# Kernel optimization log

Hardware: AMD Instinct MI355X
Metric: run time of the kernel (lower is better)

Reference implementation:

```python
import jax, jax.numpy as jnp
import numpy as np
from jax import lax

B, R, C = 4, 64, 192          # batch, input_resolution, dim
WN, K = 16, 3                 # ka_win_num, kernel_size
WS = R // 4                   # window_size = R / sqrt(WN) = 16
DN = ('NCHW', 'OIHW', 'NCHW')


def setup_inputs() -> dict:
    key = jax.random.key(0)
    ks = jax.random.split(key, 12)
    rn = lambda k, shp, s=0.05: jax.random.normal(k, shp, dtype=jnp.float32) * s
    return {
        'x': jax.random.normal(ks[0], (B, R * R, C), dtype=jnp.float32),
        'conv1_w': rn(ks[1], (WN * C, 1, K, K), 0.1),
        'dc_w': rn(ks[2], (WN, C)),                             # grouped 1x1 (WN*C -> WN)
        'dc_b': jnp.zeros((WN,), jnp.float32),
        'l1_w': rn(ks[3], (4 * WN, WN)),
        'l1_b': jnp.zeros((4 * WN,), jnp.float32),
        'l2_w': rn(ks[4], (WN, 4 * WN)),
        'l2_b': jnp.zeros((WN,), jnp.float32),
        'gk_w': rn(ks[5], (WN,)),                               # 1x1 conv WN -> 1
        'gk_b': jnp.zeros((1,), jnp.float32),
        'fusion_w': rn(ks[6], (C, (WN + 1) * C)),               # 1x1 conv (WN+1)*C -> C
        'fusion_b': jnp.zeros((C,), jnp.float32),
    }


def _forward(x, conv1_w, dc_w, dc_b, l1_w, l1_b, l2_w, l2_b, gk_w, gk_b,
             fusion_w, fusion_b):
    # pad_feature_map is a no-op since R % WS == 0.
    xw = x.reshape(B, R // WS, WS, R // WS, WS, C)
    xw = xw.transpose(0, 1, 3, 5, 2, 4).reshape(B, WN * C, WS, WS)

    # convlayer1: depthwise conv over all WN*C channels
    y = lax.conv_general_dilated(xw, conv1_w, (1, 1), [(1, 1), (1, 1)],
                                 dimension_numbers=DN,
                                 feature_group_count=WN * C)  # (B, WN*C, WS, WS)

    # WinKernel_Reweight: pool -> grouped 1x1 -> gelu -> 1x1 -> sigmoid
    pooled = y.mean(axis=(2, 3)).reshape(B, WN, C)
    w = jnp.einsum('bwc,wc->bw', pooled, dc_w) + dc_b          # downchannel (groups=WN)
    w = jax.nn.gelu(w @ l1_w.T + l1_b, approximate=False)      # (B, 4*WN)
    w = jax.nn.sigmoid(w @ l2_w.T + l2_b)                      # (B, WN)

    kern = conv1_w.reshape(WN, C, K, K)
    kern = w[:, :, None, None, None] * kern[None]              # (B, WN, C, K, K)

    # global kernel: 1x1 conv across the WN axis
    gk = jnp.einsum('bwcij,w->bcij', kern, gk_w) + gk_b[0]     # (B, C, K, K)
    all_k = jnp.concatenate([kern, gk[:, None]], axis=1)       # (B, WN+1, C, K, K)

    # dynamic depthwise conv on the full map, per sample
    xf = x.reshape(B, R, R, C).transpose(0, 3, 1, 2)           # (B, C, R, R)
    xrep = jnp.tile(xf, (1, WN + 1, 1, 1))                     # (B, (WN+1)*C, R, R)
    kflat = all_k.reshape(B, (WN + 1) * C, 1, K, K)

    def dw(xi, ki):  # xi: ((WN+1)*C, R, R), ki: ((WN+1)*C, 1, K, K)
        return lax.conv_general_dilated(xi[None], ki, (1, 1), [(1, 1), (1, 1)],
                                        dimension_numbers=DN,
                                        feature_group_count=(WN + 1) * C)[0]

    out = jax.vmap(dw)(xrep, kflat)                            # (B, (WN+1)*C, R, R)

    # fusion 1x1 conv -> (B, C, R, R) -> (B, L, C)
    out = jnp.einsum('bdhw,cd->bhwc', out, fusion_w) + fusion_b
    return out.reshape(B, R * R, C)


def reference(x, conv1_w, dc_w, dc_b, l1_w, l1_b, l2_w, l2_b, gk_w, gk_b,
              fusion_w, fusion_b):
    return _forward(x, conv1_w, dc_w, dc_b, l1_w, l1_b, l2_w, l2_b,
                    gk_w, gk_b, fusion_w, fusion_b)
```

## Files before the change

kernel.cpp:

```cpp
#include <hip/hip_runtime.h>
#include <hip/hip_bf16.h>
#include <math.h>

#define B_  4
#define R_  64
#define C_  192
#define WN_ 16


typedef __attribute__((ext_vector_type(8))) short short8;
typedef __attribute__((ext_vector_type(4))) float floatx4;

static __device__ __forceinline__ unsigned short f2bf(float f) {
    union { float f; unsigned u; } v; v.f = f;
    unsigned r = v.u + 0x7fffu + ((v.u >> 16) & 1u);
    return (unsigned short)(r >> 16);
}

__global__ __launch_bounds__(256) void pre_kernel(
        const float* __restrict__ x,
        const float* __restrict__ conv1_w,
        const float* __restrict__ dc_w,
        float* __restrict__ w0,
        unsigned short* __restrict__ xfrag,
        float* __restrict__ cw_t) {
    __shared__ float part[3];
    int blk = blockIdx.x;
    int tid = threadIdx.x;

    if (blk < 64) {
        int b = blk >> 4, win = blk & 15;
        int wr = win >> 2, wc = win & 3;
        if (tid < 192) {
            int c = tid;
            const float* xb = x + ((size_t)b * 4096) * C_ + c;
            float Wsum = 0.f, Rtop = 0.f, Rbot = 0.f, Cleft = 0.f, Cright = 0.f;
            float c00 = 0.f, c0F = 0.f, cF0 = 0.f, cFF = 0.f;
            for (int ph = 0; ph < 16; ++ph) {
                int h = wr * 16 + ph;
                #pragma unroll
                for (int pw = 0; pw < 16; ++pw) {
                    int w = wc * 16 + pw;
                    float v = xb[((size_t)(h * 64 + w)) * C_];
                    Wsum += v;
                    if (ph == 0)  { Rtop += v; if (pw == 0) c00 = v; if (pw == 15) c0F = v; }
                    if (ph == 15) { Rbot += v; if (pw == 0) cF0 = v; if (pw == 15) cFF = v; }
                    if (pw == 0)  Cleft  += v;
                    if (pw == 15) Cright += v;
                }
            }
            const float* kp = conv1_w + ((size_t)(win * C_ + c)) * 9;
            float pooled = 0.f;
            #pragma unroll
            for (int i = 0; i < 3; ++i) {
                #pragma unroll
                for (int j = 0; j < 3; ++j) {
                    int di = i - 1, dj = j - 1;
                    float S = Wsum;
                    if (di == -1) S -= Rbot;   else if (di == 1) S -= Rtop;
                    if (dj == -1) S -= Cright; else if (dj == 1) S -= Cleft;
                    if (di == -1 && dj == -1) S += cFF;
                    if (di == -1 && dj ==  1) S += cF0;
                    if (di ==  1 && dj == -1) S += c0F;
                    if (di ==  1 && dj ==  1) S += c00;
                    pooled += kp[i * 3 + j] * S;
                }
            }
            float val = (pooled * (1.f / 256.f)) * dc_w[win * C_ + c];
            for (int off = 32; off; off >>= 1) val += __shfl_down(val, off, 64);
            if ((tid & 63) == 0) part[tid >> 6] = val;
        }
        __syncthreads();
        if (tid == 0) w0[blk] = part[0] + part[1] + part[2];
    } else if (blk < 328) {
        int rb = blk - 64;
        int b = rb / 66, row = rb % 66;
        int h = row - 1;
        unsigned short* orow = xfrag + (size_t)rb * 12672;
        for (int c = tid; c < 1584; c += 256) {
            int kc = c / 264;
            int rc = c - kc * 264;
            int px = rc >> 2;
            int cio = (rc & 3) * 8;
            int w = px - 1;
            short8 o;
            if (h >= 0 && h < 64 && w >= 0 && w < 64) {
                const float* src = x + (((size_t)b * 4096) + h * 64 + w) * C_ + kc * 32 + cio;
                const float4 v0 = *(const float4*)(src);
                const float4 v1 = *(const float4*)(src + 4);
                o[0] = (short)f2bf(v0.x); o[1] = (short)f2bf(v0.y);
                o[2] = (short)f2bf(v0.z); o[3] = (short)f2bf(v0.w);
                o[4] = (short)f2bf(v1.x); o[5] = (short)f2bf(v1.y);
                o[6] = (short)f2bf(v1.z); o[7] = (short)f2bf(v1.w);
            } else {
                o = (short8){0,0,0,0,0,0,0,0};
            }
            *(short8*)(orow + (size_t)c * 8) = o;
        }
    } else {
        int base = (blk - 328) * 512 + tid * 2;
        #pragma unroll
        for (int e = 0; e < 2; ++e) {
            int o = base + e;
            int t = o / 3072;
            int r = o - t * 3072;
            cw_t[o] = conv1_w[(size_t)r * 9 + t];
        }
    }
}

__global__ __launch_bounds__(192) void weff_kernel(
        const float* __restrict__ cw_t,
        const float* __restrict__ gk_w,
        const float* __restrict__ gk_b,
        const float* __restrict__ fusion_w,
        const float* __restrict__ w0,
        const float* __restrict__ dc_b,
        const float* __restrict__ l1_w,
        const float* __restrict__ l1_b,
        const float* __restrict__ l2_w,
        const float* __restrict__ l2_b,
        unsigned short* __restrict__ Wl) {
    __shared__ float hbuf[64];
    __shared__ float s_sh[16];
    int blk = blockIdx.x;
    int b = blk / C_, co = blk % C_;
    int tid = threadIdx.x;

    if (tid < 64) {
        float a = l1_b[tid];
        #pragma unroll
        for (int w = 0; w < 16; ++w)
            a += (w0[b * 16 + w] + dc_b[w]) * l1_w[tid * 16 + w];
        hbuf[tid] = 0.5f * a * (1.f + erff(a * 0.70710678118654752f));
    }
    __syncthreads();
    if (tid < 16) {
        float a2 = l2_b[tid];
        #pragma unroll
        for (int k = 0; k < 64; ++k) a2 += hbuf[k] * l2_w[tid * 64 + k];
        s_sh[tid] = 1.f / (1.f + expf(-a2));
    }
    __syncthreads();

    int ci = tid;
    float fg = fusion_w[(size_t)co * 3264 + 16 * C_ + ci];
    float acc[9];
    float g0 = fg * gk_b[0];
    #pragma unroll
    for (int t = 0; t < 9; ++t) acc[t] = g0;
    for (int w = 0; w < 16; ++w) {
        float coef = (fusion_w[(size_t)co * 3264 + w * C_ + ci] + fg * gk_w[w]) * s_sh[w];
        #pragma unroll
        for (int t = 0; t < 9; ++t)
            acc[t] += coef * cw_t[t * 3072 + w * C_ + ci];
    }
    #pragma unroll
    for (int t = 0; t < 9; ++t) {
        int kc = ci >> 5, cio = ci & 31;
        Wl[((((size_t)(b * 9 + t)) * 6 + kc) * C_ + co) * 32 + cio] = f2bf(acc[t]);
    }
}

__global__ __launch_bounds__(256, 1) void conv_kernel(
        const unsigned short* __restrict__ xfrag,
        const unsigned short* __restrict__ Wl,
        const float* __restrict__ fusion_b,
        float* __restrict__ out) {
    const int h = blockIdx.x >> 2;
    const int b = blockIdx.x & 3;
    const int tid = threadIdx.x;
    const int wv = tid >> 6;
    const int lane = tid & 63;
    const int lo = lane & 15, quad = lane >> 4;
    const int n0 = wv * 48;

    const short* xp = (const short*)xfrag;
    const short* wp = (const short*)Wl;

    int Abase[4], Bbase[3];
    #pragma unroll
    for (int mt = 0; mt < 4; ++mt)
        Abase[mt] = (b * 66 + h + 1) * 12672 + (mt * 16 + lo + 1) * 32 + quad * 8;
    #pragma unroll
    for (int nt = 0; nt < 3; ++nt)
        Bbase[nt] = (b * 9 * 6 * C_ + n0 + nt * 16 + lo) * 32 + quad * 8;

    floatx4 acc[4][3];
    #pragma unroll
    for (int mt = 0; mt < 4; ++mt)
        #pragma unroll
        for (int nt = 0; nt < 3; ++nt)
            acc[mt][nt] = (floatx4){0.f, 0.f, 0.f, 0.f};

    short8 Ab[3][4];
    short8 Bb[3][3];

    auto load_step = [&](int s, int slot) {
        const int tap = s / 6, kc = s % 6;
        const int dh = tap / 3 - 1, dw = tap % 3 - 1;
        const int aoff = dh * 12672 + dw * 32 + kc * 2112;
        const int boff = (tap * 6 + kc) * (C_ * 32);
        #pragma unroll
        for (int mt = 0; mt < 4; ++mt)
            Ab[slot][mt] = *(const short8*)(xp + Abase[mt] + aoff);
        #pragma unroll
        for (int nt = 0; nt < 3; ++nt)
            Bb[slot][nt] = *(const short8*)(wp + Bbase[nt] + boff);
    };

    load_step(0, 0);
    load_step(1, 1);

    #pragma unroll
    for (int step = 0; step < 54; ++step) {
        const int cur = step % 3;
        if (step + 2 < 54) load_step(step + 2, (step + 2) % 3);
        #pragma unroll
        for (int mt = 0; mt < 4; ++mt)
            #pragma unroll
            for (int nt = 0; nt < 3; ++nt)
                acc[mt][nt] = __builtin_amdgcn_mfma_f32_16x16x32_bf16(
                    Ab[cur][mt], Bb[cur][nt], acc[mt][nt], 0, 0, 0);
    }

    #pragma unroll
    for (int nt = 0; nt < 3; ++nt) {
        const int co = n0 + nt * 16 + lo;
        const float fb = fusion_b[co];
        #pragma unroll
        for (int mt = 0; mt < 4; ++mt) {
            #pragma unroll
            for (int r = 0; r < 4; ++r) {
                const int pix = mt * 16 + quad * 4 + r;
                out[(((size_t)b * 4096) + h * 64 + pix) * C_ + co] = acc[mt][nt][r] + fb;
            }
        }
    }
}

extern "C" void kernel_launch(void* const* d_in, const int* in_sizes, int n_in,
                              void* d_out, int out_size, void* d_ws, size_t ws_size,
                              hipStream_t stream) {
    const float* x        = (const float*)d_in[0];
    const float* conv1_w  = (const float*)d_in[1];
    const float* dc_w     = (const float*)d_in[2];
    const float* dc_b     = (const float*)d_in[3];
    const float* l1_w     = (const float*)d_in[4];
    const float* l1_b     = (const float*)d_in[5];
    const float* l2_w     = (const float*)d_in[6];
    const float* l2_b     = (const float*)d_in[7];
    const float* gk_w     = (const float*)d_in[8];
    const float* gk_b     = (const float*)d_in[9];
    const float* fusion_w = (const float*)d_in[10];
    const float* fusion_b = (const float*)d_in[11];
    float* out = (float*)d_out;

    char* ws = (char*)d_ws;
    float* w0   = (float*)ws;
    float* cw_t = (float*)(ws + 512);
    unsigned short* Wl    = (unsigned short*)(ws + 512 + 110592);
    unsigned short* xfrag = (unsigned short*)(ws + 512 + 110592 + 2654208);

    hipLaunchKernelGGL(pre_kernel, dim3(382), dim3(256), 0, stream,
                       x, conv1_w, dc_w, w0, xfrag, cw_t);
    hipLaunchKernelGGL(weff_kernel, dim3(B_ * C_), dim3(192), 0, stream,
                       cw_t, gk_w, gk_b, fusion_w, w0, dc_b, l1_w, l1_b, l2_w, l2_b, Wl);
    hipLaunchKernelGGL(conv_kernel, dim3(R_ * B_), dim3(256), 0, stream,
                       xfrag, Wl, fusion_b, out);
}
```

Before: 126.6 us.

## Fuse bf16 input staging into conv kernel via LDS and split pooling blocks

Removes the padded bf16 xfrag workspace that pre_kernel wrote, so the conv kernel now converts three input rows from fp32 to bf16 into shared memory itself, in two channel phases. The conv block grows to 512 threads, with 8 waves split across pixel halves and channel groups, and a swizzled block-to-row mapping. The window pooling is split across 4x more blocks, and partial sums are reduced in weff_kernel. This drops a global write and read round trip and raises pooling parallelism, but adds redundant fp32 row loads (each row read by 3 blocks) and LDS barriers.

Result: faster. 120.6 us (-4.7%).

```diff
diff --git a/kernel.cpp b/kernel.cpp
--- a/kernel.cpp
+++ b/kernel.cpp
@@ -21,35 +21,34 @@
         const float* __restrict__ x,
         const float* __restrict__ conv1_w,
         const float* __restrict__ dc_w,
-        float* __restrict__ w0,
-        unsigned short* __restrict__ xfrag,
+        float* __restrict__ w0p,
         float* __restrict__ cw_t) {
     __shared__ float part[3];
     int blk = blockIdx.x;
     int tid = threadIdx.x;
 
-    if (blk < 64) {
-        int b = blk >> 4, win = blk & 15;
+    if (blk < 256) {
+        int b = blk >> 6, rest = blk & 63, win = rest >> 2, q = rest & 3;
         int wr = win >> 2, wc = win & 3;
         if (tid < 192) {
-            int c = tid;
-            const float* xb = x + ((size_t)b * 4096) * C_ + c;
+            const float* xb = x + ((size_t)b * 4096) * C_ + tid;
             float Wsum = 0.f, Rtop = 0.f, Rbot = 0.f, Cleft = 0.f, Cright = 0.f;
             float c00 = 0.f, c0F = 0.f, cF0 = 0.f, cFF = 0.f;
-            for (int ph = 0; ph < 16; ++ph) {
-                int h = wr * 16 + ph;
+            #pragma unroll
+            for (int pr = 0; pr < 4; ++pr) {
+                int h = wr * 16 + q * 4 + pr;
                 #pragma unroll
                 for (int pw = 0; pw < 16; ++pw) {
                     int w = wc * 16 + pw;
-                    float v = xb[((size_t)(h * 64 + w)) * C_];
+                    float v = xb[(size_t)(h * 64 + w) * C_];
                     Wsum += v;
-                    if (ph == 0)  { Rtop += v; if (pw == 0) c00 = v; if (pw == 15) c0F = v; }
-                    if (ph == 15) { Rbot += v; if (pw == 0) cF0 = v; if (pw == 15) cFF = v; }
+                    if (q == 0 && pr == 0) { Rtop += v; if (pw == 0) c00 = v; if (pw == 15) c0F = v; }
+                    if (q == 3 && pr == 3) { Rbot += v; if (pw == 0) cF0 = v; if (pw == 15) cFF = v; }
                     if (pw == 0)  Cleft  += v;
                     if (pw == 15) Cright += v;
                 }
             }
-            const float* kp = conv1_w + ((size_t)(win * C_ + c)) * 9;
+            const float* kp = conv1_w + ((size_t)(win * C_ + tid)) * 9;
             float pooled = 0.f;
             #pragma unroll
             for (int i = 0; i < 3; ++i) {
@@ -66,42 +65,17 @@
                     pooled += kp[i * 3 + j] * S;
                 }
             }
-            float val = (pooled * (1.f / 256.f)) * dc_w[win * C_ + c];
+            float val = (pooled * (1.f / 256.f)) * dc_w[win * C_ + tid];
             for (int off = 32; off; off >>= 1) val += __shfl_down(val, off, 64);
             if ((tid & 63) == 0) part[tid >> 6] = val;
         }
         __syncthreads();
-        if (tid == 0) w0[blk] = part[0] + part[1] + part[2];
-    } else if (blk < 328) {
-        int rb = blk - 64;
-        int b = rb / 66, row = rb % 66;
-        int h = row - 1;
-        unsigned short* orow = xfrag + (size_t)rb * 12672;
-        for (int c = tid; c < 1584; c += 256) {
-            int kc = c / 264;
-            int rc = c - kc * 264;
-            int px = rc >> 2;
-            int cio = (rc & 3) * 8;
-            int w = px - 1;
-            short8 o;
-            if (h >= 0 && h < 64 && w >= 0 && w < 64) {
-                const float* src = x + (((size_t)b * 4096) + h * 64 + w) * C_ + kc * 32 + cio;
-                const float4 v0 = *(const float4*)(src);
-                const float4 v1 = *(const float4*)(src + 4);
-                o[0] = (short)f2bf(v0.x); o[1] = (short)f2bf(v0.y);
-                o[2] = (short)f2bf(v0.z); o[3] = (short)f2bf(v0.w);
-                o[4] = (short)f2bf(v1.x); o[5] = (short)f2bf(v1.y);
-                o[6] = (short)f2bf(v1.z); o[7] = (short)f2bf(v1.w);
-            } else {
-                o = (short8){0,0,0,0,0,0,0,0};
-            }
-            *(short8*)(orow + (size_t)c * 8) = o;
-        }
+        if (tid == 0) w0p[blk] = part[0] + part[1] + part[2];
     } else {
-        int base = (blk - 328) * 512 + tid * 2;
+        int basei = (blk - 256) * 512 + tid * 2;
         #pragma unroll
         for (int e = 0; e < 2; ++e) {
-            int o = base + e;
+            int o = basei + e;
             int t = o / 3072;
             int r = o - t * 3072;
             cw_t[o] = conv1_w[(size_t)r * 9 + t];
@@ -114,7 +88,7 @@
         const float* __restrict__ gk_w,
         const float* __restrict__ gk_b,
         const float* __restrict__ fusion_w,
-        const float* __restrict__ w0,
+        const float* __restrict__ w0p,
         const float* __restrict__ dc_b,
         const float* __restrict__ l1_w,
         const float* __restrict__ l1_b,
@@ -130,8 +104,11 @@
     if (tid < 64) {
         float a = l1_b[tid];
         #pragma unroll
-        for (int w = 0; w < 16; ++w)
-            a += (w0[b * 16 + w] + dc_b[w]) * l1_w[tid * 16 + w];
+        for (int w = 0; w < 16; ++w) {
+            float w0 = w0p[b * 64 + w * 4 + 0] + w0p[b * 64 + w * 4 + 1]
+                     + w0p[b * 64 + w * 4 + 2] + w0p[b * 64 + w * 4 + 3];
+            a += (w0 + dc_b[w]) * l1_w[tid * 16 + w];
+        }
         hbuf[tid] = 0.5f * a * (1.f + erff(a * 0.70710678118654752f));
     }
     __syncthreads();
@@ -162,66 +139,103 @@
     }
 }
 
-__global__ __launch_bounds__(256, 1) void conv_kernel(
-        const unsigned short* __restrict__ xfrag,
+__global__ __launch_bounds__(512, 2) void conv_kernel(
+        const float* __restrict__ x,
         const unsigned short* __restrict__ Wl,
         const float* __restrict__ fusion_b,
         float* __restrict__ out) {
-    const int h = blockIdx.x >> 2;
-    const int b = blockIdx.x & 3;
+    __shared__ unsigned short Asm[3 * 3 * 66 * 32];
+    const int n = blockIdx.x;
+    const int g = (n & 7) * 32 + (n >> 3);
+    const int b = g >> 6, h = g & 63;
     const int tid = threadIdx.x;
-    const int wv = tid >> 6;
-    const int lane = tid & 63;
+    const int wv = tid >> 6, lane = tid & 63;
     const int lo = lane & 15, quad = lane >> 4;
-    const int n0 = wv * 48;
-
-    const short* xp = (const short*)xfrag;
+    const int cs = wv >> 1, pxh = wv & 1;
+    const int n0 = cs * 48;
+
     const short* wp = (const short*)Wl;
-
-    int Abase[4], Bbase[3];
-    #pragma unroll
-    for (int mt = 0; mt < 4; ++mt)
-        Abase[mt] = (b * 66 + h + 1) * 12672 + (mt * 16 + lo + 1) * 32 + quad * 8;
+    int Bbase[3];
     #pragma unroll
     for (int nt = 0; nt < 3; ++nt)
-        Bbase[nt] = (b * 9 * 6 * C_ + n0 + nt * 16 + lo) * 32 + quad * 8;
-
-    floatx4 acc[4][3];
-    #pragma unroll
-    for (int mt = 0; mt < 4; ++mt)
+        Bbase[nt] = (b * 54 * C_ + n0 + nt * 16 + lo) * 32 + quad * 8;
+    int Alds[2];
+    #pragma unroll
+    for (int mt = 0; mt < 2; ++mt)
+        Alds[mt] = (pxh * 32 + mt * 16 + lo + 1) * 32 + quad * 8;
+
+    floatx4 acc[2][3];
+    #pragma unroll
+    for (int mt = 0; mt < 2; ++mt)
         #pragma unroll
         for (int nt = 0; nt < 3; ++nt)
             acc[mt][nt] = (floatx4){0.f, 0.f, 0.f, 0.f};
 
-    short8 Ab[3][4];
-    short8 Bb[3][3];
-
-    auto load_step = [&](int s, int slot) {
-        const int tap = s / 6, kc = s % 6;
-        const int dh = tap / 3 - 1, dw = tap % 3 - 1;
-        const int aoff = dh * 12672 + dw * 32 + kc * 2112;
-        const int boff = (tap * 6 + kc) * (C_ * 32);
-        #pragma unroll
-        for (int mt = 0; mt < 4; ++mt)
-            Ab[slot][mt] = *(const short8*)(xp + Abase[mt] + aoff);
-        #pragma unroll
-        for (int nt = 0; nt < 3; ++nt)
-            Bb[slot][nt] = *(const short8*)(wp + Bbase[nt] + boff);
-    };
-
-    load_step(0, 0);
-    load_step(1, 1);
-
-    #pragma unroll
-    for (int step = 0; step < 54; ++step) {
-        const int cur = step % 3;
-        if (step + 2 < 54) load_step(step + 2, (step + 2) % 3);
-        #pragma unroll
-        for (int mt = 0; mt < 4; ++mt)
+    #pragma unroll
+    for (int ph = 0; ph < 2; ++ph) {
+        const int kc0 = ph * 3;
+        #pragma unroll
+        for (int r = 0; r < 3; ++r) {
+            int hr = h - 1 + r;
+            unsigned short* Lr = Asm + r * (3 * 66 * 32);
+            if (hr >= 0 && hr < 64) {
+                const float* src = x + ((size_t)(b * 4096 + hr * 64)) * C_ + kc0 * 32;
+                for (int c = tid; c < 768; c += 512) {
+                    int px = c / 12, sub = c % 12;
+                    int kcl = sub >> 2, ci0 = (sub & 3) * 8;
+                    const float* p = src + px * C_ + kcl * 32 + ci0;
+                    float4 v0 = *(const float4*)p;
+                    float4 v1 = *(const float4*)(p + 4);
+                    short8 o;
+                    o[0] = (short)f2bf(v0.x); o[1] = (short)f2bf(v0.y);
+                    o[2] = (short)f2bf(v0.z); o[3] = (short)f2bf(v0.w);
+                    o[4] = (short)f2bf(v1.x); o[5] = (short)f2bf(v1.y);
+                    o[6] = (short)f2bf(v1.z); o[7] = (short)f2bf(v1.w);
+                    *(short8*)(Lr + (kcl * 66 + px + 1) * 32 + ci0) = o;
+                }
+            } else {
+                for (int c = tid; c < 792; c += 512)
+                    *(short8*)(Lr + c * 8) = (short8){0, 0, 0, 0, 0, 0, 0, 0};
+            }
+        }
+        if (tid < 72) {
+            int loc = tid >> 2, j = tid & 3;
+            int r = loc / 6, rem = loc % 6, kcl = rem >> 1, px = (rem & 1) * 65;
+            *(short8*)(Asm + ((r * 3 + kcl) * 66 + px) * 32 + j * 8) =
+                (short8){0, 0, 0, 0, 0, 0, 0, 0};
+        }
+        __syncthreads();
+
+        short8 Bb[3][3], Ab[2][2];
+        auto loadB = [&](int t27, int slot) {
+            int tap = t27 / 3, kcl = t27 % 3;
+            int s = tap * 6 + kc0 + kcl;
             #pragma unroll
             for (int nt = 0; nt < 3; ++nt)
-                acc[mt][nt] = __builtin_amdgcn_mfma_f32_16x16x32_bf16(
-                    Ab[cur][mt], Bb[cur][nt], acc[mt][nt], 0, 0, 0);
+                Bb[slot][nt] = *(const short8*)(wp + Bbase[nt] + s * (C_ * 32));
+        };
+        auto loadA = [&](int t27, int slot) {
+            int tap = t27 / 3, kcl = t27 % 3;
+            int dh = tap / 3, dw = tap % 3 - 1;
+            int base = ((dh * 3 + kcl) * 66 + dw) * 32;
+            #pragma unroll
+            for (int mt = 0; mt < 2; ++mt)
+                Ab[slot][mt] = *(const short8*)((const short*)Asm + base + Alds[mt]);
+        };
+        loadB(0, 0); loadB(1, 1); loadA(0, 0);
+        #pragma unroll
+        for (int t = 0; t < 27; ++t) {
+            const int bc = t % 3, ac = t & 1;
+            if (t + 2 < 27) loadB(t + 2, (t + 2) % 3);
+            if (t + 1 < 27) loadA(t + 1, ac ^ 1);
+            #pragma unroll
+            for (int mt = 0; mt < 2; ++mt)
+                #pragma unroll
+                for (int nt = 0; nt < 3; ++nt)
+                    acc[mt][nt] = __builtin_amdgcn_mfma_f32_16x16x32_bf16(
+                        Ab[ac][mt], Bb[bc][nt], acc[mt][nt], 0, 0, 0);
+        }
+        __syncthreads();
     }
 
     #pragma unroll
@@ -229,11 +243,11 @@
         const int co = n0 + nt * 16 + lo;
         const float fb = fusion_b[co];
         #pragma unroll
-        for (int mt = 0; mt < 4; ++mt) {
+        for (int mt = 0; mt < 2; ++mt) {
             #pragma unroll
             for (int r = 0; r < 4; ++r) {
-                const int pix = mt * 16 + quad * 4 + r;
-                out[(((size_t)b * 4096) + h * 64 + pix) * C_ + co] = acc[mt][nt][r] + fb;
+                const int px = pxh * 32 + mt * 16 + quad * 4 + r;
+                out[((size_t)(b * 4096 + h * 64 + px)) * C_ + co] = acc[mt][nt][r] + fb;
             }
         }
     }
@@ -257,15 +271,14 @@
     float* out = (float*)d_out;
 
     char* ws = (char*)d_ws;
-    float* w0   = (float*)ws;
-    float* cw_t = (float*)(ws + 512);
-    unsigned short* Wl    = (unsigned short*)(ws + 512 + 110592);
-    unsigned short* xfrag = (unsigned short*)(ws + 512 + 110592 + 2654208);
-
-    hipLaunchKernelGGL(pre_kernel, dim3(382), dim3(256), 0, stream,
-                       x, conv1_w, dc_w, w0, xfrag, cw_t);
+    float* w0p  = (float*)ws;
+    float* cw_t = (float*)(ws + 1024);
+    unsigned short* Wl = (unsigned short*)(ws + 1024 + 110592);
+
+    hipLaunchKernelGGL(pre_kernel, dim3(310), dim3(256), 0, stream,
+                       x, conv1_w, dc_w, w0p, cw_t);
     hipLaunchKernelGGL(weff_kernel, dim3(B_ * C_), dim3(192), 0, stream,
-                       cw_t, gk_w, gk_b, fusion_w, w0, dc_b, l1_w, l1_b, l2_w, l2_b, Wl);
-    hipLaunchKernelGGL(conv_kernel, dim3(R_ * B_), dim3(256), 0, stream,
-                       xfrag, Wl, fusion_b, out);
-}
+                       cw_t, gk_w, gk_b, fusion_w, w0p, dc_b, l1_w, l1_b, l2_w, l2_b, Wl);
+    hipLaunchKernelGGL(conv_kernel, dim3(256), dim3(512), 0, stream,
+                       x, Wl, fusion_b, out);
+}
```
